# Performance work log

Measured on AMD Instinct MI355X. Metric: run time of the kernel, lower is better.

Reference implementation:

```python
import jax, jax.numpy as jnp
import numpy as np

N, E, F_IN, DIM, G = 50000, 800000, 128, 128, 512
NUM_GC_LAYERS = 3
S2S_STEPS = 3


def setup_inputs() -> dict:
    key = jax.random.key(0)
    ks = jax.random.split(key, 17)
    s = 0.05
    rn = lambda k, shape: jax.random.normal(k, shape, jnp.float32) * s
    x = jax.random.normal(ks[0], (N, F_IN), jnp.float32)
    edge_index = jax.random.randint(ks[1], (2, E), 0, N)
    batch = jnp.sort(jax.random.randint(ks[2], (N,), 0, G))
    return dict(
        x=x, edge_index=edge_index, batch=batch,
        lin0_W=rn(ks[3], (DIM, F_IN)), lin0_b=rn(ks[4], (DIM,)),
        gin_W1=rn(ks[5], (DIM, DIM)), gin_b1=rn(ks[6], (DIM,)),
        gin_W2=rn(ks[7], (DIM, DIM)), gin_b2=rn(ks[8], (DIM,)),
        gru_Wih=rn(ks[9], (3 * DIM, DIM)), gru_Whh=rn(ks[10], (3 * DIM, DIM)),
        gru_bih=rn(ks[11], (3 * DIM,)), gru_bhh=rn(ks[12], (3 * DIM,)),
        lstm_Wih=rn(ks[13], (4 * DIM, 2 * DIM)), lstm_Whh=rn(ks[14], (4 * DIM, DIM)),
        lstm_bih=rn(ks[15], (4 * DIM,)), lstm_bhh=rn(ks[16], (4 * DIM,)),
    )


def reference(x, edge_index, batch, lin0_W, lin0_b, gin_W1, gin_b1, gin_W2, gin_b2,
              gru_Wih, gru_Whh, gru_bih, gru_bhh,
              lstm_Wih, lstm_Whh, lstm_bih, lstm_bhh):
    src, dst = edge_index[0], edge_index[1]
    out = jax.nn.relu(x @ lin0_W.T + lin0_b)          # [N, DIM]
    h = out                                            # GRU hidden (seq_len=1, 1 layer)
    for _ in range(NUM_GC_LAYERS):
        # GINConv, eps=0: nn(x + sum_{j in N(i)} x_j); scatter-add over edge list
        aggr = jax.ops.segment_sum(out[src], dst, num_segments=N)
        z = out + aggr
        m = jax.nn.relu(jax.nn.relu(z @ gin_W1.T + gin_b1) @ gin_W2.T + gin_b2)
        # single GRU step (PyTorch gate order: r, z, n)
        gx = m @ gru_Wih.T + gru_bih
        gh = h @ gru_Whh.T + gru_bhh
        gxr, gxz, gxn = jnp.split(gx, 3, axis=-1)
        ghr, ghz, ghn = jnp.split(gh, 3, axis=-1)
        r = jax.nn.sigmoid(gxr + ghr)
        zt = jax.nn.sigmoid(gxz + ghz)
        n = jnp.tanh(gxn + r * ghn)
        h = (1.0 - zt) * n + zt * h
        out = h
    # Set2Set pooling (processing_steps=3), LSTM(2*DIM -> DIM), gate order i,f,g,o
    q_star = jnp.zeros((G, 2 * DIM), x.dtype)
    hl = jnp.zeros((G, DIM), x.dtype)
    cl = jnp.zeros((G, DIM), x.dtype)
    for _ in range(S2S_STEPS):
        gates = q_star @ lstm_Wih.T + lstm_bih + hl @ lstm_Whh.T + lstm_bhh
        i, f, g, o = jnp.split(gates, 4, axis=-1)
        cl = jax.nn.sigmoid(f) * cl + jax.nn.sigmoid(i) * jnp.tanh(g)
        hl = jax.nn.sigmoid(o) * jnp.tanh(cl)
        q = hl                                          # [G, DIM]
        e = jnp.sum(out * q[batch], axis=-1)            # [N] attention logits
        emax = jax.lax.stop_gradient(jax.ops.segment_max(e, batch, num_segments=G))
        emax = jnp.where(jnp.isfinite(emax), emax, 0.0)
        a_num = jnp.exp(e - emax[batch])
        denom = jax.ops.segment_sum(a_num, batch, num_segments=G)
        a = a_num / (denom[batch] + 1e-16)              # per-graph softmax
        rvec = jax.ops.segment_sum(a[:, None] * out, batch, num_segments=G)
        q_star = jnp.concatenate([q, rvec], axis=-1)    # [G, 2*DIM]
    return (q_star, out)
```

## Files before the change

kernel.cpp:

```cpp
#include <hip/hip_runtime.h>
#include <hip/hip_bf16.h>
#include <math.h>

static constexpr int NN  = 50000;
static constexpr int NE  = 800000;
static constexpr int DIM = 128;
static constexpr int NG  = 512;
static constexpr int NBLK = (NN + 255) / 256;

typedef __attribute__((ext_vector_type(8))) short bf16x8;
typedef __attribute__((ext_vector_type(4))) float f32x4;

__device__ __forceinline__ float sigm(float x) {
    return __builtin_amdgcn_rcpf(1.0f + __expf(-x));
}
__device__ __forceinline__ float ftanh(float x) {
    x = fminf(fmaxf(x, -15.f), 15.f);
    float t = __expf(2.f * x);
    return (t - 1.f) * __builtin_amdgcn_rcpf(t + 1.f);
}
__device__ __forceinline__ float b2f(ushort u) { return __uint_as_float(((unsigned)u) << 16); }
__device__ __forceinline__ ushort f2b(float f) {
    __hip_bfloat16 h = __float2bfloat16(f);
    return *reinterpret_cast<ushort*>(&h);
}
__device__ __forceinline__ bf16x8 ldb8(const ushort* p) {
    return *reinterpret_cast<const bf16x8*>(p);
}

__global__ __launch_bounds__(256) void k_prep(const float* __restrict__ lin0_W,
                                              const float* __restrict__ gin_W1,
                                              const float* __restrict__ gin_W2,
                                              const float* __restrict__ gru_Wih,
                                              const float* __restrict__ gru_Whh,
                                              const float* __restrict__ gru_bih,
                                              const float* __restrict__ gru_bhh,
                                              const float* __restrict__ lstm_Wih,
                                              const float* __restrict__ lstm_Whh,
                                              const float* __restrict__ lstm_bih,
                                              const float* __restrict__ lstm_bhh,
                                              const int* __restrict__ batch,
                                              ushort* __restrict__ wlin0,
                                              ushort* __restrict__ wg1,
                                              ushort* __restrict__ wg2,
                                              ushort* __restrict__ wihb,
                                              ushort* __restrict__ whhb,
                                              ushort* __restrict__ wrz,
                                              float* __restrict__ brz,
                                              float* __restrict__ wltr,
                                              float* __restrict__ bl,
                                              int* __restrict__ deg,
                                              int* __restrict__ gstart,
                                              float* __restrict__ zf) {
    const int S0 = 16384, S1 = S0 + 16384, S2 = S1 + 16384;
    const int S3 = S2 + 49152, S4 = S3 + 49152, S5 = S4 + 65536;
    const int S6 = S5 + 256, S7 = S6 + 196608, S8 = S7 + 512;
    const int S9 = S8 + (NN + 1), S10 = S9 + (NG + 1), S11 = S10 + 262144;
    int i = blockIdx.x * 256 + threadIdx.x;
    if (i < S0) { wlin0[i] = f2b(lin0_W[i]); }
    else if (i < S1) { int j = i - S0; wg1[j] = f2b(gin_W1[j]); }
    else if (i < S2) { int j = i - S1; wg2[j] = f2b(gin_W2[j]); }
    else if (i < S3) { int j = i - S2; wihb[j] = f2b(gru_Wih[j]); }
    else if (i < S4) { int j = i - S3; whhb[j] = f2b(gru_Whh[j]); }
    else if (i < S5) {
        int j = i - S4; int col = j >> 8, k = j & 255;
        int row = (col >> 7) * 128 + (col & 127);
        wrz[j] = f2b((k < 128) ? gru_Whh[row * 128 + k] : gru_Wih[row * 128 + (k - 128)]);
    }
    else if (i < S6) { int j = i - S5; brz[j] = gru_bih[j] + gru_bhh[j]; }
    else if (i < S7) {
        int j = i - S6; int k = j / 512, col = j % 512;
        wltr[j] = (k < 256) ? lstm_Wih[(size_t)col * 256 + k]
                            : lstm_Whh[(size_t)col * 128 + (k - 256)];
    }
    else if (i < S8) { int j = i - S7; bl[j] = lstm_bih[j] + lstm_bhh[j]; }
    else if (i < S9) { deg[i - S8] = 0; }
    else if (i < S10) {
        int g = i - S9;
        int lo = 0, hi = NN;
        while (lo < hi) { int mid = (lo + hi) >> 1; if (batch[mid] < g) lo = mid + 1; else hi = mid; }
        gstart[g] = lo;
    }
    else if (i < S11) { zf[i - S10] = 0.f; }
}
static constexpr int PREP_TOTAL = 16384 * 3 + 49152 * 2 + 65536 + 256 + 196608 + 512 + (NN + 1) + (NG + 1) + 262144;

__global__ void k_count(const int* __restrict__ dst, int* __restrict__ deg, int e) {
    int i = blockIdx.x * blockDim.x + threadIdx.x;
    if (i < e) atomicAdd(&deg[dst[i]], 1);
}

__global__ __launch_bounds__(256) void k_scan_blk(const int* __restrict__ deg,
                                                  int* __restrict__ part,
                                                  int* __restrict__ blksum) {
    __shared__ int s[256];
    int b = blockIdx.x, t = threadIdx.x;
    int i = b * 256 + t;
    int v = (i < NN) ? deg[i] : 0;
    s[t] = v;
    __syncthreads();
    #pragma unroll
    for (int off = 1; off < 256; off <<= 1) {
        int x = (t >= off) ? s[t - off] : 0;
        __syncthreads();
        s[t] += x;
        __syncthreads();
    }
    if (i < NN) part[i] = s[t] - v;
    if (t == 255) blksum[b] = s[255];
}
__global__ __launch_bounds__(256) void k_scan_top(const int* __restrict__ blksum,
                                                  int* __restrict__ blkoff) {
    __shared__ int s[256];
    int t = threadIdx.x;
    int v = (t < NBLK) ? blksum[t] : 0;
    s[t] = v;
    __syncthreads();
    #pragma unroll
    for (int off = 1; off < 256; off <<= 1) {
        int x = (t >= off) ? s[t - off] : 0;
        __syncthreads();
        s[t] += x;
        __syncthreads();
    }
    if (t < NBLK) blkoff[t] = s[t] - v;
    if (t == NBLK - 1) blkoff[NBLK] = s[t];
}
__global__ __launch_bounds__(256) void k_scan_add(const int* __restrict__ part,
                                                  const int* __restrict__ blkoff,
                                                  int* __restrict__ rowptr,
                                                  int* __restrict__ bcur) {
    int b = blockIdx.x, t = threadIdx.x;
    int i = b * 256 + t;
    if (i < NN) {
        int r = part[i] + blkoff[b];
        rowptr[i] = r;
        if ((i & 255) == 0) bcur[i >> 8] = r;
    }
    if (b == 0 && t == 0) rowptr[NN] = blkoff[NBLK];
}

__global__ __launch_bounds__(256) void k_bucket(const int* __restrict__ src,
                                                const int* __restrict__ dst,
                                                int* __restrict__ bcur,
                                                int2* __restrict__ pairs, int e) {
    __shared__ int lcnt[256];
    __shared__ int lbase[256];
    int tid = threadIdx.x;
    lcnt[tid] = 0;
    __syncthreads();
    int base = blockIdx.x * 4096;
    #pragma unroll
    for (int k = 0; k < 16; ++k) {
        int e0 = base + k * 256 + tid;
        if (e0 < e) atomicAdd(&lcnt[dst[e0] >> 8], 1);
    }
    __syncthreads();
    int cnt = lcnt[tid];
    if (cnt > 0) lbase[tid] = atomicAdd(&bcur[tid], cnt);
    __syncthreads();
    lcnt[tid] = 0;
    __syncthreads();
    #pragma unroll
    for (int k = 0; k < 16; ++k) {
        int e0 = base + k * 256 + tid;
        if (e0 < e) {
            int d = dst[e0];
            int b = d >> 8;
            int off = atomicAdd(&lcnt[b], 1);
            pairs[lbase[b] + off] = make_int2(src[e0], d);
        }
    }
}
__global__ __launch_bounds__(256) void k_fillbkt(const int2* __restrict__ pairs,
                                                 const int* __restrict__ rowptr,
                                                 int* __restrict__ csr) {
    __shared__ int lcur[256];
    int b = blockIdx.x, tid = threadIdx.x;
    int w0 = b << 8;
    int w1 = min(w0 + 256, NN);
    if (w0 + tid < w1) lcur[tid] = rowptr[w0 + tid];
    __syncthreads();
    int r0 = rowptr[w0], r1 = rowptr[w1];
    for (int i = r0 + tid; i < r1; i += 256) {
        int2 p = pairs[i];
        int pos = atomicAdd(&lcur[p.y - w0], 1);
        csr[pos] = p.x;
    }
}

__global__ __launch_bounds__(256) void k_aggr8(const ushort* __restrict__ AB,
                                               const int* __restrict__ rowptr,
                                               const int* __restrict__ csr,
                                               ushort* __restrict__ Z) {
    int node = blockIdx.x * 4 + (threadIdx.x >> 6);
    if (node >= NN) return;
    int lane = threadIdx.x & 63;
    const unsigned* base = (const unsigned*)AB;
    unsigned u = base[(size_t)node * 64 + lane];
    float s0a = b2f(u & 0xffff), s0b = b2f(u >> 16);
    float s1a = 0.f, s1b = 0.f, s2a = 0.f, s2b = 0.f, s3a = 0.f, s3b = 0.f;
    float s4a = 0.f, s4b = 0.f, s5a = 0.f, s5b = 0.f, s6a = 0.f, s6b = 0.f, s7a = 0.f, s7b = 0.f;
    int p = rowptr[node], p1 = rowptr[node + 1];
    for (; p + 8 <= p1; p += 8) {
        unsigned v0 = base[(size_t)csr[p + 0] * 64 + lane];
        unsigned v1 = base[(size_t)csr[p + 1] * 64 + lane];
        unsigned v2 = base[(size_t)csr[p + 2] * 64 + lane];
        unsigned v3 = base[(size_t)csr[p + 3] * 64 + lane];
        unsigned v4 = base[(size_t)csr[p + 4] * 64 + lane];
        unsigned v5 = base[(size_t)csr[p + 5] * 64 + lane];
        unsigned v6 = base[(size_t)csr[p + 6] * 64 + lane];
        unsigned v7 = base[(size_t)csr[p + 7] * 64 + lane];
        s0a += b2f(v0 & 0xffff); s0b += b2f(v0 >> 16);
        s1a += b2f(v1 & 0xffff); s1b += b2f(v1 >> 16);
        s2a += b2f(v2 & 0xffff); s2b += b2f(v2 >> 16);
        s3a += b2f(v3 & 0xffff); s3b += b2f(v3 >> 16);
        s4a += b2f(v4 & 0xffff); s4b += b2f(v4 >> 16);
        s5a += b2f(v5 & 0xffff); s5b += b2f(v5 >> 16);
        s6a += b2f(v6 & 0xffff); s6b += b2f(v6 >> 16);
        s7a += b2f(v7 & 0xffff); s7b += b2f(v7 >> 16);
    }
    for (; p < p1; ++p) {
        unsigned v = base[(size_t)csr[p] * 64 + lane];
        s0a += b2f(v & 0xffff); s0b += b2f(v >> 16);
    }
    s0a += (s1a + s2a) + (s3a + s4a) + (s5a + s6a) + s7a;
    s0b += (s1b + s2b) + (s3b + s4b) + (s5b + s6b) + s7b;
    unsigned o = ((unsigned)f2b(s0b) << 16) | (unsigned)f2b(s0a);
    ((unsigned*)(Z + (size_t)node * 128))[lane] = o;
}

__global__ __launch_bounds__(256) void k_lin0(const float* __restrict__ X,
                                              const ushort* __restrict__ W,
                                              const float* __restrict__ bias,
                                              ushort* __restrict__ AB, int n) {
    int lane = threadIdx.x & 63, wave = threadIdx.x >> 6;
    int c0 = lane & 15, kg = (lane >> 4) * 8;
    int tb0 = wave * 32;
    bf16x8 B[2][4];
    #pragma unroll
    for (int t = 0; t < 2; ++t)
        #pragma unroll
        for (int kk = 0; kk < 4; ++kk)
            B[t][kk] = ldb8(W + (size_t)(tb0 + t * 16 + c0) * 128 + kk * 32 + kg);

    for (int m0 = blockIdx.x * 64; m0 < n; m0 += gridDim.x * 64) {
        f32x4 acc[4][2];
        #pragma unroll
        for (int m = 0; m < 4; ++m) { acc[m][0] = {0,0,0,0}; acc[m][1] = {0,0,0,0}; }
        #pragma unroll
        for (int kk = 0; kk < 4; ++kk) {
            #pragma unroll
            for (int m = 0; m < 4; ++m) {
                int ar = min(m0 + m * 16 + c0, n - 1);
                const float* a = X + (size_t)ar * 128 + kk * 32 + kg;
                float4 x0 = *reinterpret_cast<const float4*>(a);
                float4 x1 = *reinterpret_cast<const float4*>(a + 4);
                bf16x8 af;
                af[0] = (short)f2b(x0.x); af[1] = (short)f2b(x0.y);
                af[2] = (short)f2b(x0.z); af[3] = (short)f2b(x0.w);
                af[4] = (short)f2b(x1.x); af[5] = (short)f2b(x1.y);
                af[6] = (short)f2b(x1.z); af[7] = (short)f2b(x1.w);
                acc[m][0] = __builtin_amdgcn_mfma_f32_16x16x32_bf16(af, B[0][kk], acc[m][0], 0, 0, 0);
                acc[m][1] = __builtin_amdgcn_mfma_f32_16x16x32_bf16(af, B[1][kk], acc[m][1], 0, 0, 0);
            }
        }
        #pragma unroll
        for (int m = 0; m < 4; ++m) {
            int rbase = m0 + m * 16 + ((lane >> 4) << 2);
            #pragma unroll
            for (int t = 0; t < 2; ++t) {
                int col = tb0 + t * 16 + c0;
                float bv = bias[col];
                #pragma unroll
                for (int j = 0; j < 4; ++j) {
                    int row = rbase + j;
                    if (row < n) {
                        float v = fmaxf(acc[m][t][j] + bv, 0.f);
                        AB[(size_t)row * 128 + col] = f2b(v);
                    }
                }
            }
        }
    }
}

__global__ __launch_bounds__(512) void k_ginmlp3(const ushort* __restrict__ Zt,
                                                 const ushort* __restrict__ W1,
                                                 const float* __restrict__ b1,
                                                 const ushort* __restrict__ W2,
                                                 const float* __restrict__ b2,
                                                 ushort* __restrict__ mt, int n) {
    __shared__ ushort Z_lds[32 * 136];
    __shared__ ushort M_lds[32 * 136];
    int tid = threadIdx.x;
    int lane = tid & 63, wave = tid >> 6;
    int c0 = lane & 15, kg = (lane >> 4) * 8;
    int colw = wave * 16 + c0;
    int rj = (lane >> 4) << 2;
    int srow = tid >> 4, scol = (tid & 15) * 8;
    const int stride = gridDim.x * 32;

    bf16x8 B1[4], B2[4];
    #pragma unroll
    for (int kk = 0; kk < 4; ++kk) {
        B1[kk] = ldb8(W1 + (size_t)colw * 128 + kk * 32 + kg);
        B2[kk] = ldb8(W2 + (size_t)colw * 128 + kk * 32 + kg);
    }
    float bv1 = b1[colw], bv2 = b2[colw];

    int m0 = blockIdx.x * 32;
    bf16x8 pz;
    if (m0 < n) pz = ldb8(Zt + (size_t)min(m0 + srow, n - 1) * 128 + scol);
    for (; m0 < n; m0 += stride) {
        *reinterpret_cast<bf16x8*>(&Z_lds[srow * 136 + scol]) = pz;
        __syncthreads();
        int mn = m0 + stride;
        if (mn < n) pz = ldb8(Zt + (size_t)min(mn + srow, n - 1) * 128 + scol);
        {
            f32x4 a[2] = {{0,0,0,0},{0,0,0,0}};
            #pragma unroll
            for (int kk = 0; kk < 4; ++kk) {
                bf16x8 f0 = *reinterpret_cast<const bf16x8*>(&Z_lds[c0 * 136 + kk * 32 + kg]);
                bf16x8 f1 = *reinterpret_cast<const bf16x8*>(&Z_lds[(16 + c0) * 136 + kk * 32 + kg]);
                a[0] = __builtin_amdgcn_mfma_f32_16x16x32_bf16(f0, B1[kk], a[0], 0, 0, 0);
                a[1] = __builtin_amdgcn_mfma_f32_16x16x32_bf16(f1, B1[kk], a[1], 0, 0, 0);
            }
            #pragma unroll
            for (int m = 0; m < 2; ++m)
                #pragma unroll
                for (int j = 0; j < 4; ++j)
                    M_lds[(m * 16 + rj + j) * 136 + colw] = f2b(fmaxf(a[m][j] + bv1, 0.f));
        }
        __syncthreads();
        {
            f32x4 a[2] = {{0,0,0,0},{0,0,0,0}};
            #pragma unroll
            for (int kk = 0; kk < 4; ++kk) {
                bf16x8 f0 = *reinterpret_cast<const bf16x8*>(&M_lds[c0 * 136 + kk * 32 + kg]);
                bf16x8 f1 = *reinterpret_cast<const bf16x8*>(&M_lds[(16 + c0) * 136 + kk * 32 + kg]);
                a[0] = __builtin_amdgcn_mfma_f32_16x16x32_bf16(f0, B2[kk], a[0], 0, 0, 0);
                a[1] = __builtin_amdgcn_mfma_f32_16x16x32_bf16(f1, B2[kk], a[1], 0, 0, 0);
            }
            #pragma unroll
            for (int m = 0; m < 2; ++m)
                #pragma unroll
                for (int j = 0; j < 4; ++j) {
                    int grow = m0 + m * 16 + rj + j;
                    if (grow < n)
                        mt[(size_t)grow * 128 + colw] = f2b(fmaxf(a[m][j] + bv2, 0.f));
                }
        }
        __syncthreads();
    }
}

template<bool WRITEH>
__global__ __launch_bounds__(512) void k_gru3b(const ushort* __restrict__ ABin,
                                               const ushort* __restrict__ mt,
                                               const ushort* __restrict__ wrz,
                                               const float* __restrict__ brz,
                                               const ushort* __restrict__ Wn,
                                               const ushort* __restrict__ Un,
                                               const float* __restrict__ bin,
                                               const float* __restrict__ bhn,
                                               float* __restrict__ Hf,
                                               ushort* __restrict__ ABout, int n) {
    __shared__ ushort A_lds[32 * 264];
    int tid = threadIdx.x;
    int lane = tid & 63, wave = tid >> 6;
    int c0 = lane & 15, kg = (lane >> 4) * 8;
    int colw = wave * 16 + c0;
    int rj = (lane >> 4) << 2;
    int srow = tid >> 4, scol = (tid & 15) * 8;
    const int stride = gridDim.x * 32;

    bf16x8 Brz[2][8];
    #pragma unroll
    for (int kk = 0; kk < 8; ++kk) {
        Brz[0][kk] = ldb8(wrz + (size_t)(colw) * 256 + kk * 32 + kg);
        Brz[1][kk] = ldb8(wrz + (size_t)(128 + colw) * 256 + kk * 32 + kg);
    }
    bf16x8 Bn[4], Bu[4];
    #pragma unroll
    for (int kk = 0; kk < 4; ++kk) {
        Bn[kk] = ldb8(Wn + (size_t)colw * 128 + kk * 32 + kg);
        Bu[kk] = ldb8(Un + (size_t)colw * 128 + kk * 32 + kg);
    }
    float biN = bin[colw], bhN = bhn[colw];
    float brzR = brz[colw], brzZ = brz[128 + colw];

    int m0 = blockIdx.x * 32;
    bf16x8 ph, pm;
    if (m0 < n) {
        int gr = min(m0 + srow, n - 1);
        ph = ldb8(ABin + (size_t)gr * 128 + scol);
        pm = ldb8(mt + (size_t)gr * 128 + scol);
    }
    for (; m0 < n; m0 += stride) {
        *reinterpret_cast<bf16x8*>(&A_lds[srow * 264 + scol]) = ph;
        *reinterpret_cast<bf16x8*>(&A_lds[srow * 264 + 128 + scol]) = pm;
        __syncthreads();
        int mn = m0 + stride;
        if (mn < n) {
            int gr = min(mn + srow, n - 1);
            ph = ldb8(ABin + (size_t)gr * 128 + scol);
            pm = ldb8(mt + (size_t)gr * 128 + scol);
        }
        f32x4 aR[2] = {{0,0,0,0},{0,0,0,0}};
        f32x4 aZ[2] = {{0,0,0,0},{0,0,0,0}};
        #pragma unroll
        for (int kk = 0; kk < 8; ++kk) {
            bf16x8 f0 = *reinterpret_cast<const bf16x8*>(&A_lds[c0 * 264 + kk * 32 + kg]);
            bf16x8 f1 = *reinterpret_cast<const bf16x8*>(&A_lds[(16 + c0) * 264 + kk * 32 + kg]);
            aR[0] = __builtin_amdgcn_mfma_f32_16x16x32_bf16(f0, Brz[0][kk], aR[0], 0, 0, 0);
            aZ[0] = __builtin_amdgcn_mfma_f32_16x16x32_bf16(f0, Brz[1][kk], aZ[0], 0, 0, 0);
            aR[1] = __builtin_amdgcn_mfma_f32_16x16x32_bf16(f1, Brz[0][kk], aR[1], 0, 0, 0);
            aZ[1] = __builtin_amdgcn_mfma_f32_16x16x32_bf16(f1, Brz[1][kk], aZ[1], 0, 0, 0);
        }
        f32x4 an[2] = {{0,0,0,0},{0,0,0,0}};
        f32x4 au[2] = {{0,0,0,0},{0,0,0,0}};
        #pragma unroll
        for (int kk = 0; kk < 4; ++kk) {
            bf16x8 am0 = *reinterpret_cast<const bf16x8*>(&A_lds[c0 * 264 + 128 + kk * 32 + kg]);
            bf16x8 ah0 = *reinterpret_cast<const bf16x8*>(&A_lds[c0 * 264 + kk * 32 + kg]);
            bf16x8 am1 = *reinterpret_cast<const bf16x8*>(&A_lds[(16 + c0) * 264 + 128 + kk * 32 + kg]);
            bf16x8 ah1 = *reinterpret_cast<const bf16x8*>(&A_lds[(16 + c0) * 264 + kk * 32 + kg]);
            an[0] = __builtin_amdgcn_mfma_f32_16x16x32_bf16(am0, Bn[kk], an[0], 0, 0, 0);
            au[0] = __builtin_amdgcn_mfma_f32_16x16x32_bf16(ah0, Bu[kk], au[0], 0, 0, 0);
            an[1] = __builtin_amdgcn_mfma_f32_16x16x32_bf16(am1, Bn[kk], an[1], 0, 0, 0);
            au[1] = __builtin_amdgcn_mfma_f32_16x16x32_bf16(ah1, Bu[kk], au[1], 0, 0, 0);
        }
        #pragma unroll
        for (int m = 0; m < 2; ++m)
            #pragma unroll
            for (int j = 0; j < 4; ++j) {
                int row = m * 16 + rj + j;
                int grow = m0 + row;
                if (grow < n) {
                    float r  = sigm(aR[m][j] + brzR);
                    float zt = sigm(aZ[m][j] + brzZ);
                    float hold = b2f(A_lds[row * 264 + colw]);
                    float nn = ftanh(an[m][j] + biN + r * (au[m][j] + bhN));
                    float hn = (1.f - zt) * nn + zt * hold;
                    ABout[(size_t)grow * 128 + colw] = f2b(hn);
                    if (WRITEH) Hf[(size_t)grow * 128 + colw] = hn;
                }
            }
        __syncthreads();
    }
}

__global__ __launch_bounds__(512) void k_s2s(const ushort* __restrict__ AB,
                                             const float* __restrict__ Wt,
                                             const float* __restrict__ bl,
                                             const int* __restrict__ gstart,
                                             const float* __restrict__ qstar,
                                             float* __restrict__ hl,
                                             float* __restrict__ cl,
                                             float* __restrict__ qout) {
    int g = blockIdx.x, tid = threadIdx.x, lane = tid & 63, wave = tid >> 6;
    __shared__ float qh[384];
    __shared__ float gbuf[512];
    __shared__ float q[128];
    __shared__ float wm[8];
    __shared__ float sw[8];
    __shared__ float rv[8][128];
    if (tid < 256) qh[tid] = qstar[(size_t)g * 256 + tid];
    else if (tid < 384) qh[tid] = hl[(size_t)g * 128 + (tid - 256)];
    __syncthreads();
    float acc = bl[tid];
    #pragma unroll 8
    for (int k = 0; k < 384; ++k)
        acc += Wt[(size_t)k * 512 + tid] * qh[k];
    gbuf[tid] = acc;
    __syncthreads();
    if (tid < 128) {
        float iv = sigm(gbuf[tid]);
        float fv = sigm(gbuf[128 + tid]);
        float gv = ftanh(gbuf[256 + tid]);
        float ov = sigm(gbuf[384 + tid]);
        float cn = fv * cl[(size_t)g * 128 + tid] + iv * gv;
        cl[(size_t)g * 128 + tid] = cn;
        float hn = ov * ftanh(cn);
        hl[(size_t)g * 128 + tid] = hn;
        q[tid] = hn;
    }
    __syncthreads();
    int s = gstart[g], e = gstart[g + 1];
    float q0 = q[2 * lane], q1 = q[2 * lane + 1];
    float mx = -1e30f, sumw = 0.f, a0 = 0.f, a1 = 0.f;
    for (int node = s + wave; node < e; node += 8) {
        unsigned u = ((const unsigned*)AB)[(size_t)node * 64 + lane];
        float v0 = b2f(u & 0xffff), v1 = b2f(u >> 16);
        float p = v0 * q0 + v1 * q1;
        #pragma unroll
        for (int off = 1; off < 64; off <<= 1) p += __shfl_xor(p, off);
        float nm = fmaxf(mx, p);
        float corr = __expf(mx - nm);
        float wgt = __expf(p - nm);
        sumw = sumw * corr + wgt;
        a0 = a0 * corr + wgt * v0;
        a1 = a1 * corr + wgt * v1;
        mx = nm;
    }
    if (lane == 0) wm[wave] = mx;
    __syncthreads();
    float gm = fmaxf(fmaxf(fmaxf(wm[0], wm[1]), fmaxf(wm[2], wm[3])),
                     fmaxf(fmaxf(wm[4], wm[5]), fmaxf(wm[6], wm[7])));
    float cw = __expf(mx - gm);
    rv[wave][2 * lane] = a0 * cw;
    rv[wave][2 * lane + 1] = a1 * cw;
    if (lane == 0) sw[wave] = sumw * cw;
    __syncthreads();
    if (tid < 128) {
        float r = 0.f, d = 1e-16f;
        #pragma unroll
        for (int wv = 0; wv < 8; ++wv) r += rv[wv][tid];
        #pragma unroll
        for (int wv = 0; wv < 8; ++wv) d += sw[wv];
        qout[(size_t)g * 256 + tid] = q[tid];
        qout[(size_t)g * 256 + 128 + tid] = r / d;
    }
}

extern "C" void kernel_launch(void* const* d_in, const int* in_sizes, int n_in,
                              void* d_out, int out_size, void* d_ws, size_t ws_size,
                              hipStream_t stream) {
    const float* x        = (const float*)d_in[0];
    const int*   ei       = (const int*)d_in[1];
    const int*   batch    = (const int*)d_in[2];
    const float* lin0_W   = (const float*)d_in[3];
    const float* lin0_b   = (const float*)d_in[4];
    const float* gin_W1   = (const float*)d_in[5];
    const float* gin_b1   = (const float*)d_in[6];
    const float* gin_W2   = (const float*)d_in[7];
    const float* gin_b2   = (const float*)d_in[8];
    const float* gru_Wih  = (const float*)d_in[9];
    const float* gru_Whh  = (const float*)d_in[10];
    const float* gru_bih  = (const float*)d_in[11];
    const float* gru_bhh  = (const float*)d_in[12];
    const float* lstm_Wih = (const float*)d_in[13];
    const float* lstm_Whh = (const float*)d_in[14];
    const float* lstm_bih = (const float*)d_in[15];
    const float* lstm_bhh = (const float*)d_in[16];

    float* qstar_out = (float*)d_out;
    float* h         = (float*)d_out + (size_t)NG * 2 * DIM;

    char* w = (char*)d_ws;
    ushort* AB0   = (ushort*)w; w += (size_t)NN * 128 * 2;
    ushort* AB1   = (ushort*)w; w += (size_t)NN * 128 * 2;
    ushort* zt    = (ushort*)w; w += (size_t)NN * 128 * 2;
    ushort* mt    = (ushort*)w; w += (size_t)NN * 128 * 2;
    ushort* wlin0 = (ushort*)w; w += 16384 * 2;
    ushort* wg1   = (ushort*)w; w += 16384 * 2;
    ushort* wg2   = (ushort*)w; w += 16384 * 2;
    ushort* wihb  = (ushort*)w; w += 49152 * 2;
    ushort* whhb  = (ushort*)w; w += 49152 * 2;
    ushort* wrz   = (ushort*)w; w += 65536 * 2;
    float* brz    = (float*)w;  w += 256 * 4;
    float* wltr   = (float*)w;  w += (size_t)512 * 384 * 4;
    float* bl     = (float*)w;  w += 512 * 4;
    float* qstar  = (float*)w;  w += (size_t)NG * 2 * DIM * 4;
    float* hl     = (float*)w;  w += (size_t)NG * DIM * 4;
    float* cl     = (float*)w;  w += (size_t)NG * DIM * 4;
    int* deg      = (int*)w;    w += (size_t)(NN + 1) * 4;
    int* rowptr   = (int*)w;    w += (size_t)(NN + 1) * 4;
    int* bcur     = (int*)w;    w += 256 * 4;
    int* csr_src  = (int*)w;    w += (size_t)NE * 4;
    int2* pairs   = (int2*)w;   w += (size_t)NE * 8;
    int* gstart   = (int*)w;    w += (size_t)(NG + 1) * 4;
    int* part     = (int*)w;    w += (size_t)NN * 4;
    int* blksum   = (int*)w;    w += (size_t)(NBLK + 1) * 4;
    int* blkoff   = (int*)w;    w += (size_t)(NBLK + 1) * 4;

    const int* src = ei;
    const int* dst = ei + NE;

    k_prep<<<(PREP_TOTAL + 255) / 256, 256, 0, stream>>>(
        lin0_W, gin_W1, gin_W2, gru_Wih, gru_Whh, gru_bih, gru_bhh,
        lstm_Wih, lstm_Whh, lstm_bih, lstm_bhh, batch,
        wlin0, wg1, wg2, wihb, whhb, wrz, brz, wltr, bl, deg, gstart, qstar);

    k_count<<<(NE + 255) / 256, 256, 0, stream>>>(dst, deg, NE);
    k_scan_blk<<<NBLK, 256, 0, stream>>>(deg, part, blksum);
    k_scan_top<<<1, 256, 0, stream>>>(blksum, blkoff);
    k_scan_add<<<NBLK, 256, 0, stream>>>(part, blkoff, rowptr, bcur);
    k_bucket<<<(NE + 4095) / 4096, 256, 0, stream>>>(src, dst, bcur, pairs, NE);
    k_fillbkt<<<NBLK, 256, 0, stream>>>(pairs, rowptr, csr_src);

    k_lin0<<<782, 256, 0, stream>>>(x, wlin0, lin0_b, AB0, NN);

    for (int t = 0; t < 3; ++t) {
        ushort* ABc = (t & 1) ? AB1 : AB0;
        ushort* ABn = (t & 1) ? AB0 : AB1;
        k_aggr8<<<(NN + 3) / 4, 256, 0, stream>>>(ABc, rowptr, csr_src, zt);
        k_ginmlp3<<<1024, 512, 0, stream>>>(zt, wg1, gin_b1, wg2, gin_b2, mt, NN);
        if (t < 2)
            k_gru3b<false><<<512, 512, 0, stream>>>(ABc, mt, wrz, brz,
                                                    wihb + 256 * 128, whhb + 256 * 128,
                                                    gru_bih + 256, gru_bhh + 256, h, ABn, NN);
        else
            k_gru3b<true><<<512, 512, 0, stream>>>(ABc, mt, wrz, brz,
                                                   wihb + 256 * 128, whhb + 256 * 128,
                                                   gru_bih + 256, gru_bhh + 256, h, ABn, NN);
    }
    const ushort* ABfin = AB1;

    for (int st = 0; st < 3; ++st)
        k_s2s<<<NG, 512, 0, stream>>>(ABfin, wltr, bl, gstart, qstar, hl, cl,
                                      (st == 2) ? qstar_out : qstar);
}
```

Baseline: 408.5 us.

## Fuse neighbor aggregation into GIN MLP kernel, dropping intermediate Z buffer

Replaces the separate gather-sum kernel and GIN MLP kernel with one kernel where each block gathers neighbor rows for 32 nodes directly into LDS, using 16 threads per row with 16-byte loads, then runs the two MFMA layers. This removes a full write and read of the N x 128 bf16 intermediate and one launch per layer. In exchange the gather parallelism drops (16 lanes per node, 4-way unroll vs 64 lanes, 8-way) and the prefetch of the next tile is lost, so gather latency is no longer overlapped with the MFMA stage.

Result: faster. 398.7 us (-2.4%).

```diff
diff --git a/kernel.cpp b/kernel.cpp
--- a/kernel.cpp
+++ b/kernel.cpp
@@ -10,6 +10,7 @@
 
 typedef __attribute__((ext_vector_type(8))) short bf16x8;
 typedef __attribute__((ext_vector_type(4))) float f32x4;
+typedef __attribute__((ext_vector_type(8))) float f32x8;
 
 __device__ __forceinline__ float sigm(float x) {
     return __builtin_amdgcn_rcpf(1.0f + __expf(-x));
@@ -26,6 +27,13 @@
 }
 __device__ __forceinline__ bf16x8 ldb8(const ushort* p) {
     return *reinterpret_cast<const bf16x8*>(p);
+}
+__device__ __forceinline__ f32x8 acc8(f32x8 a, uint4 v) {
+    a[0] += b2f(v.x & 0xffff); a[1] += b2f(v.x >> 16);
+    a[2] += b2f(v.y & 0xffff); a[3] += b2f(v.y >> 16);
+    a[4] += b2f(v.z & 0xffff); a[5] += b2f(v.z >> 16);
+    a[6] += b2f(v.w & 0xffff); a[7] += b2f(v.w >> 16);
+    return a;
 }
 
 __global__ __launch_bounds__(256) void k_prep(const float* __restrict__ lin0_W,
@@ -189,47 +197,6 @@
     }
 }
 
-__global__ __launch_bounds__(256) void k_aggr8(const ushort* __restrict__ AB,
-                                               const int* __restrict__ rowptr,
-                                               const int* __restrict__ csr,
-                                               ushort* __restrict__ Z) {
-    int node = blockIdx.x * 4 + (threadIdx.x >> 6);
-    if (node >= NN) return;
-    int lane = threadIdx.x & 63;
-    const unsigned* base = (const unsigned*)AB;
-    unsigned u = base[(size_t)node * 64 + lane];
-    float s0a = b2f(u & 0xffff), s0b = b2f(u >> 16);
-    float s1a = 0.f, s1b = 0.f, s2a = 0.f, s2b = 0.f, s3a = 0.f, s3b = 0.f;
-    float s4a = 0.f, s4b = 0.f, s5a = 0.f, s5b = 0.f, s6a = 0.f, s6b = 0.f, s7a = 0.f, s7b = 0.f;
-    int p = rowptr[node], p1 = rowptr[node + 1];
-    for (; p + 8 <= p1; p += 8) {
-        unsigned v0 = base[(size_t)csr[p + 0] * 64 + lane];
-        unsigned v1 = base[(size_t)csr[p + 1] * 64 + lane];
-        unsigned v2 = base[(size_t)csr[p + 2] * 64 + lane];
-        unsigned v3 = base[(size_t)csr[p + 3] * 64 + lane];
-        unsigned v4 = base[(size_t)csr[p + 4] * 64 + lane];
-        unsigned v5 = base[(size_t)csr[p + 5] * 64 + lane];
-        unsigned v6 = base[(size_t)csr[p + 6] * 64 + lane];
-        unsigned v7 = base[(size_t)csr[p + 7] * 64 + lane];
-        s0a += b2f(v0 & 0xffff); s0b += b2f(v0 >> 16);
-        s1a += b2f(v1 & 0xffff); s1b += b2f(v1 >> 16);
-        s2a += b2f(v2 & 0xffff); s2b += b2f(v2 >> 16);
-        s3a += b2f(v3 & 0xffff); s3b += b2f(v3 >> 16);
-        s4a += b2f(v4 & 0xffff); s4b += b2f(v4 >> 16);
-        s5a += b2f(v5 & 0xffff); s5b += b2f(v5 >> 16);
-        s6a += b2f(v6 & 0xffff); s6b += b2f(v6 >> 16);
-        s7a += b2f(v7 & 0xffff); s7b += b2f(v7 >> 16);
-    }
-    for (; p < p1; ++p) {
-        unsigned v = base[(size_t)csr[p] * 64 + lane];
-        s0a += b2f(v & 0xffff); s0b += b2f(v >> 16);
-    }
-    s0a += (s1a + s2a) + (s3a + s4a) + (s5a + s6a) + s7a;
-    s0b += (s1b + s2b) + (s3b + s4b) + (s5b + s6b) + s7b;
-    unsigned o = ((unsigned)f2b(s0b) << 16) | (unsigned)f2b(s0a);
-    ((unsigned*)(Z + (size_t)node * 128))[lane] = o;
-}
-
 __global__ __launch_bounds__(256) void k_lin0(const float* __restrict__ X,
                                               const ushort* __restrict__ W,
                                               const float* __restrict__ bias,
@@ -285,12 +252,14 @@
     }
 }
 
-__global__ __launch_bounds__(512) void k_ginmlp3(const ushort* __restrict__ Zt,
-                                                 const ushort* __restrict__ W1,
-                                                 const float* __restrict__ b1,
-                                                 const ushort* __restrict__ W2,
-                                                 const float* __restrict__ b2,
-                                                 ushort* __restrict__ mt, int n) {
+__global__ __launch_bounds__(512) void k_aggmlp(const ushort* __restrict__ AB,
+                                                const int* __restrict__ rowptr,
+                                                const int* __restrict__ csr,
+                                                const ushort* __restrict__ W1,
+                                                const float* __restrict__ b1,
+                                                const ushort* __restrict__ W2,
+                                                const float* __restrict__ b2,
+                                                ushort* __restrict__ mt, int n) {
     __shared__ ushort Z_lds[32 * 136];
     __shared__ ushort M_lds[32 * 136];
     int tid = threadIdx.x;
@@ -298,7 +267,8 @@
     int c0 = lane & 15, kg = (lane >> 4) * 8;
     int colw = wave * 16 + c0;
     int rj = (lane >> 4) << 2;
-    int srow = tid >> 4, scol = (tid & 15) * 8;
+    int grow_r = tid >> 4;
+    int segi = tid & 15;
     const int stride = gridDim.x * 32;
 
     bf16x8 B1[4], B2[4];
@@ -308,15 +278,32 @@
         B2[kk] = ldb8(W2 + (size_t)colw * 128 + kk * 32 + kg);
     }
     float bv1 = b1[colw], bv2 = b2[colw];
-
-    int m0 = blockIdx.x * 32;
-    bf16x8 pz;
-    if (m0 < n) pz = ldb8(Zt + (size_t)min(m0 + srow, n - 1) * 128 + scol);
-    for (; m0 < n; m0 += stride) {
-        *reinterpret_cast<bf16x8*>(&Z_lds[srow * 136 + scol]) = pz;
-        __syncthreads();
-        int mn = m0 + stride;
-        if (mn < n) pz = ldb8(Zt + (size_t)min(mn + srow, n - 1) * 128 + scol);
+    const uint4* bp = (const uint4*)AB;
+
+    for (int m0 = blockIdx.x * 32; m0 < n; m0 += stride) {
+        f32x8 A0 = {0,0,0,0,0,0,0,0};
+        int grow = m0 + grow_r;
+        if (grow < n) {
+            f32x8 A1 = {0,0,0,0,0,0,0,0}, A2 = {0,0,0,0,0,0,0,0}, A3 = {0,0,0,0,0,0,0,0};
+            A0 = acc8(A0, bp[(size_t)grow * 16 + segi]);
+            int p = rowptr[grow], p1 = rowptr[grow + 1];
+            for (; p + 4 <= p1; p += 4) {
+                uint4 v0 = bp[(size_t)csr[p + 0] * 16 + segi];
+                uint4 v1 = bp[(size_t)csr[p + 1] * 16 + segi];
+                uint4 v2 = bp[(size_t)csr[p + 2] * 16 + segi];
+                uint4 v3 = bp[(size_t)csr[p + 3] * 16 + segi];
+                A0 = acc8(A0, v0); A1 = acc8(A1, v1);
+                A2 = acc8(A2, v2); A3 = acc8(A3, v3);
+            }
+            for (; p < p1; ++p) A0 = acc8(A0, bp[(size_t)csr[p] * 16 + segi]);
+            #pragma unroll
+            for (int i = 0; i < 8; ++i) A0[i] += A1[i] + A2[i] + A3[i];
+        }
+        bf16x8 zz;
+        #pragma unroll
+        for (int i = 0; i < 8; ++i) zz[i] = (short)f2b(A0[i]);
+        *reinterpret_cast<bf16x8*>(&Z_lds[grow_r * 136 + segi * 8]) = zz;
+        __syncthreads();
         {
             f32x4 a[2] = {{0,0,0,0},{0,0,0,0}};
             #pragma unroll
@@ -346,9 +333,9 @@
             for (int m = 0; m < 2; ++m)
                 #pragma unroll
                 for (int j = 0; j < 4; ++j) {
-                    int grow = m0 + m * 16 + rj + j;
-                    if (grow < n)
-                        mt[(size_t)grow * 128 + colw] = f2b(fmaxf(a[m][j] + bv2, 0.f));
+                    int gr2 = m0 + m * 16 + rj + j;
+                    if (gr2 < n)
+                        mt[(size_t)gr2 * 128 + colw] = f2b(fmaxf(a[m][j] + bv2, 0.f));
                 }
         }
         __syncthreads();
@@ -551,7 +538,6 @@
     char* w = (char*)d_ws;
     ushort* AB0   = (ushort*)w; w += (size_t)NN * 128 * 2;
     ushort* AB1   = (ushort*)w; w += (size_t)NN * 128 * 2;
-    ushort* zt    = (ushort*)w; w += (size_t)NN * 128 * 2;
     ushort* mt    = (ushort*)w; w += (size_t)NN * 128 * 2;
     ushort* wlin0 = (ushort*)w; w += 16384 * 2;
     ushort* wg1   = (ushort*)w; w += 16384 * 2;
@@ -595,8 +581,8 @@
     for (int t = 0; t < 3; ++t) {
         ushort* ABc = (t & 1) ? AB1 : AB0;
         ushort* ABn = (t & 1) ? AB0 : AB1;
-        k_aggr8<<<(NN + 3) / 4, 256, 0, stream>>>(ABc, rowptr, csr_src, zt);
-        k_ginmlp3<<<1024, 512, 0, stream>>>(zt, wg1, gin_b1, wg2, gin_b2, mt, NN);
+        k_aggmlp<<<1024, 512, 0, stream>>>(ABc, rowptr, csr_src,
+                                           wg1, gin_b1, wg2, gin_b2, mt, NN);
         if (t < 2)
             k_gru3b<false><<<512, 512, 0, stream>>>(ABc, mt, wrz, brz,
                                                     wihb + 256 * 128, whhb + 256 * 128,
```
